# Kernel tuning notes

Measured on AMD Instinct MI355X. Metric: run time of the kernel, lower is better.

The kernel has to match this reference:

```python
import jax, jax.numpy as jnp
import numpy as np

BATCH, N_BEADS, BEAD_SIZE, N_ATOMS = 32, 16384, 16, 100000
INV_SQRT2 = 0.7071067811865476  # e3nn 'uuu' 1o x 1o -> 1e (irrep_normalization='none') cross-product scale


def _mask_arrays():
    # Deterministic bead->atom mask: bead h places count_h = (h % 16) + 1 atoms.
    counts = np.arange(N_BEADS) % BEAD_SIZE + 1
    mask = np.arange(BEAD_SIZE)[None, :] < counts[:, None]  # (n_beads, bead_size)
    slot_idx = np.nonzero(mask.ravel())[0].astype(np.int32)  # flat positions of True entries, (M,)
    bead_idx = np.repeat(np.arange(N_BEADS), counts).astype(np.int32)  # bead id per placed atom, (M,)
    return slot_idx, bead_idx


def setup_inputs() -> dict:
    slot_idx, bead_idx = _mask_arrays()
    M = slot_idx.shape[0]  # 139264
    rng = np.random.default_rng(0)
    atom_idx = rng.integers(0, N_ATOMS, size=M).astype(np.int32)  # bead2atom_idcs flattened over beads
    key = jax.random.key(0)
    kP, k1, k2, kw, ka, ks = jax.random.split(key, 6)
    return {
        'P': jax.random.normal(kP, (BATCH, N_BEADS, 3), jnp.float32),
        'p1': jax.random.normal(k1, (BATCH, N_BEADS, 3), jnp.float32),
        'p2': jax.random.normal(k2, (BATCH, N_BEADS, 3), jnp.float32),
        'weights': jax.random.normal(kw, (3, N_BEADS, BEAD_SIZE), jnp.float32),
        'angles_polar': jax.random.normal(ka, (M, 1), jnp.float32),
        'scaling': jax.random.normal(ks, (N_ATOMS, 1), jnp.float32),
        'slot_idx': jnp.asarray(slot_idx),
        'atom_idx': jnp.asarray(atom_idx),
        'bead_idx': jnp.asarray(bead_idx),
    }


def _q_mult(q1, q2):
    w1, x1, y1, z1 = jnp.moveaxis(q1, -1, 0)
    w2, x2, y2, z2 = jnp.moveaxis(q2, -1, 0)
    w = w1 * w2 - x1 * x2 - y1 * y2 - z1 * z2
    x = w1 * x2 + x1 * w2 + y1 * z2 - z1 * y2
    y = w1 * y2 + y1 * w2 + z1 * x2 - x1 * z2
    z = w1 * z2 + z1 * w2 + x1 * y2 - y1 * x2
    return jnp.stack((w, x, y, z), -1)


def _qv_mult(q, v):
    q2 = jnp.concatenate([jnp.zeros(v.shape[:-1] + (1,), v.dtype), v], -1)
    q_conj = q * jnp.asarray([1.0, -1.0, -1.0, -1.0], q.dtype)
    return _q_mult(_q_mult(q, q2), q_conj)[..., 1:]


def reference(P, p1, p2, weights, angles_polar, scaling, slot_idx, atom_idx, bead_idx):
    B = P.shape[0]
    # per-bead cross product (e3nn TensorProduct 'uuu' path)
    p12 = jnp.cross(p1, p2) * jnp.asarray(INV_SQRT2, p1.dtype)
    stacked = jnp.stack([p1, p2, p12], axis=1)                      # (B, 3, H, 3)
    rot = jnp.einsum('bihk,ihl->bhlk', stacked, weights)            # (B, H, L, 3)
    rot = rot / jnp.linalg.norm(rot, axis=-1, keepdims=True)
    rot_flat = rot.reshape(B, N_BEADS * BEAD_SIZE, 3)[:, slot_idx]  # (B, M, 3) gather via mask
    # quaternions: real = cos(theta), imag = sin(theta) * axis
    cos_a = jnp.cos(angles_polar)                                   # (M, 1)
    sin_a = jnp.sin(angles_polar)
    q = jnp.concatenate([jnp.broadcast_to(cos_a, (B,) + cos_a.shape), sin_a[None] * rot_flat], -1)  # (B, M, 4)
    v = p1[:, bead_idx]                                             # (B, M, 3) repeat_interleave by counts
    v_rot = _qv_mult(q, v)                                          # (B, M, 3)
    recon = scaling[atom_idx][None] * v_rot + P[:, bead_idx]        # (B, M, 3)
    out = jnp.zeros((B, N_ATOMS, 3), P.dtype).at[:, atom_idx].add(recon)  # scatter-add (overlaps accumulate)
    return out, rot_flat.reshape(-1, 3)
```

## Files before the change

kernel.cpp:

```cpp
#include <hip/hip_runtime.h>
#include <hip/hip_fp16.h>
#include <math.h>

#define BATCH   32
#define N_BEADS 16384
#define BEAD_SIZE 16
#define N_ATOMS 100000
#define INV_SQRT2 0.70710678118654752440f
#define SCAN_BLK 256

typedef float v4f __attribute__((ext_vector_type(4)));

__global__ void __launch_bounds__(256)
zero_kernel(int* __restrict__ p, int n)
{
    int i = blockIdx.x * 256 + threadIdx.x;
    if (i < n) p[i] = 0;
}

__global__ void __launch_bounds__(256)
countrec_kernel(const int* __restrict__ atom_idx,
                const int* __restrict__ slot_idx,
                const float* __restrict__ W,
                const float* __restrict__ ang,
                const float* __restrict__ scal,
                int* __restrict__ counts,
                float4* __restrict__ rec1,
                float4* __restrict__ recM2, int M)
{
    int m = blockIdx.x * blockDim.x + threadIdx.x;
    if (m >= M) return;
    int a = atom_idx[m];
    atomicAdd(&counts[a], 1);
    int slot = slot_idx[m];
    int h = slot >> 4, l = slot & 15;
    float w0 = W[(0 * N_BEADS + h) * BEAD_SIZE + l];
    float w1 = W[(1 * N_BEADS + h) * BEAD_SIZE + l];
    float w2 = W[(2 * N_BEADS + h) * BEAD_SIZE + l];
    rec1[m] = make_float4(__int_as_float(slot), w0, w1, w2);
    float sa, ca;
    __sincosf(ang[m], &sa, &ca);
    recM2[m] = make_float4(2.f * ca * sa, 2.f * sa * sa, scal[a], 0.f);
}

__global__ void __launch_bounds__(SCAN_BLK)
scan1_kernel(const int* __restrict__ counts, int* __restrict__ off,
             int* __restrict__ bsum, int n)
{
    __shared__ int s[SCAN_BLK];
    int i = blockIdx.x * SCAN_BLK + threadIdx.x;
    int c = (i < n) ? counts[i] : 0;
    s[threadIdx.x] = c;
    __syncthreads();
    int v = c;
    for (int d = 1; d < SCAN_BLK; d <<= 1) {
        int t = (threadIdx.x >= d) ? s[threadIdx.x - d] : 0;
        __syncthreads();
        v += t;
        s[threadIdx.x] = v;
        __syncthreads();
    }
    if (i < n) off[i] = v - c;
    if (threadIdx.x == SCAN_BLK - 1) bsum[blockIdx.x] = v;
}

__global__ void __launch_bounds__(256)
scan3_kernel(int* __restrict__ off, const int* __restrict__ bsum,
             const int* __restrict__ counts,
             int* __restrict__ cursor2, float4* __restrict__ rec_a, int n)
{
    __shared__ int red[256];
    int j = blockIdx.x;
    int partial = 0;
    for (int i = threadIdx.x; i < j; i += 256) partial += bsum[i];
    red[threadIdx.x] = partial;
    __syncthreads();
    for (int d = 128; d > 0; d >>= 1) {
        if ((int)threadIdx.x < d) red[threadIdx.x] += red[threadIdx.x + d];
        __syncthreads();
    }
    int bpref = red[0];
    int i = j * 256 + threadIdx.x;
    if (i >= n) return;
    int o = off[i] + bpref;
    off[i] = o;
    cursor2[i] = o;
    rec_a[i] = make_float4(__int_as_float(counts[i]), __int_as_float(o),
                           0.f, 0.f);
}

__global__ void __launch_bounds__(256)
fill3_kernel(const int* __restrict__ atom_idx,
             int* __restrict__ cursor2, int* __restrict__ csr_m, int M)
{
    int m = blockIdx.x * blockDim.x + threadIdx.x;
    if (m >= M) return;
    int pos = atomicAdd(&cursor2[atom_idx[m]], 1);
    csr_m[pos] = m;
}

__global__ void __launch_bounds__(256)
mcontrib_kernel(const float4* __restrict__ rec1,
                const float4* __restrict__ recM2,
                const float* __restrict__ p1,
                const float* __restrict__ p2,
                const float* __restrict__ P,
                float* __restrict__ out_rot,
                uint2* __restrict__ cM16,
                int M)
{
    int bg = blockIdx.y;
    int mbase = blockIdx.x * 256;
    int m = mbase + threadIdx.x;
    int b0 = bg * 4;
    bool act = m < M;
    int mc = act ? m : (M - 1);

    float4 r1 = rec1[mc];
    float4 r2 = recM2[mc];
    int h = __float_as_int(r1.x) >> 4;
    float A = r2.x, Bc = r2.y, s = r2.z;
    size_t hoff = (size_t)h * 3;

    __shared__ float sbuf[768];
    int nm = M - mbase; if (nm > 256) nm = 256;
    int nf = nm * 3;
    int nf4 = nf >> 2;
    int done = nf4 << 2;
    int rem = nf - done;

#pragma unroll
    for (int i = 0; i < 4; ++i) {
        int b = b0 + i;
        const size_t bb = (size_t)b * N_BEADS * 3;
        const float* p1p = p1 + bb + hoff;
        const float* p2p = p2 + bb + hoff;
        const float* Pp  = P  + bb + hoff;
        float a1x = p1p[0], a1y = p1p[1], a1z = p1p[2];
        float a2x = p2p[0], a2y = p2p[1], a2z = p2p[2];

        float cxx = (a1y * a2z - a1z * a2y) * INV_SQRT2;
        float cyy = (a1z * a2x - a1x * a2z) * INV_SQRT2;
        float czz = (a1x * a2y - a1y * a2x) * INV_SQRT2;
        float rx = r1.y * a1x + r1.z * a2x + r1.w * cxx;
        float ry = r1.y * a1y + r1.z * a2y + r1.w * cyy;
        float rz = r1.y * a1z + r1.z * a2z + r1.w * czz;
        float inv = rsqrtf(rx * rx + ry * ry + rz * rz);
        rx *= inv; ry *= inv; rz *= inv;

        __syncthreads();
        sbuf[threadIdx.x * 3 + 0] = rx;
        sbuf[threadIdx.x * 3 + 1] = ry;
        sbuf[threadIdx.x * 3 + 2] = rz;
        __syncthreads();
        {
            size_t base = ((size_t)b * M + mbase) * 3;
            v4f* dst = (v4f*)(out_rot + base);
            if ((base & 3) == 0) {
                if ((int)threadIdx.x < nf4)
                    __builtin_nontemporal_store(
                        ((const v4f*)sbuf)[threadIdx.x], &dst[threadIdx.x]);
                if ((int)threadIdx.x < rem)
                    __builtin_nontemporal_store(
                        sbuf[done + threadIdx.x], &out_rot[base + done + threadIdx.x]);
            } else if (act) {
                out_rot[base + threadIdx.x * 3 + 0] = rx;
                out_rot[base + threadIdx.x * 3 + 1] = ry;
                out_rot[base + threadIdx.x * 3 + 2] = rz;
            }
        }

        float ux = ry * a1z - rz * a1y;
        float uy = rz * a1x - rx * a1z;
        float uz = rx * a1y - ry * a1x;
        float wx = ry * uz - rz * uy;
        float wy = rz * ux - rx * uz;
        float wz = rx * uy - ry * ux;
        float ox = s * (a1x + A * ux + Bc * wx) + Pp[0];
        float oy = s * (a1y + A * uy + Bc * wy) + Pp[1];
        float oz = s * (a1z + A * uz + Bc * wz) + Pp[2];

        if (act) {
            union { struct { __half2 lo, hi; } hh; uint2 u; } pk;
            pk.hh.lo = __floats2half2_rn(ox, oy);
            pk.hh.hi = __floats2half2_rn(oz, 0.f);
            cM16[(size_t)b * M + m] = pk.u;
        }
    }
}

__global__ void __launch_bounds__(256)
sum2_kernel(const float4* __restrict__ rec_a,
            const int* __restrict__ csr_m,
            const uint2* __restrict__ cM16,
            float* __restrict__ out_atoms, int M, int abps)
{
    int beta = blockIdx.x;
    int xcd  = beta & 7;
    int j    = beta >> 3;
    int round = j / abps;
    int ablk  = j - round * abps;
    int b = xcd + 8 * round;
    int abase = ablk * 256;
    int a = abase + threadIdx.x;

    float ax = 0.f, ay = 0.f, az = 0.f;
    if (a < N_ATOMS) {
        float4 ra = rec_a[a];
        int cnt = __float_as_int(ra.x);
        int o   = __float_as_int(ra.y);
        const uint2* cb = cM16 + (size_t)b * M;
        for (int k = 0; k < cnt; ++k) {
            int m = csr_m[o + k];
            union { uint2 u; struct { __half2 lo, hi; } hh; } pk;
            pk.u = cb[m];
            float2 xy = __half22float2(pk.hh.lo);
            float2 zp = __half22float2(pk.hh.hi);
            ax += xy.x; ay += xy.y; az += zp.x;
        }
    }
    __shared__ float sbuf[768];
    sbuf[threadIdx.x * 3 + 0] = ax;
    sbuf[threadIdx.x * 3 + 1] = ay;
    sbuf[threadIdx.x * 3 + 2] = az;
    __syncthreads();

    int na = N_ATOMS - abase; if (na > 256) na = 256;
    int nf = na * 3;
    size_t base = ((size_t)b * N_ATOMS + abase) * 3;
    int nf4 = nf >> 2;
    v4f* dst = (v4f*)(out_atoms + base);
    if ((int)threadIdx.x < nf4)
        __builtin_nontemporal_store(((const v4f*)sbuf)[threadIdx.x],
                                    &dst[threadIdx.x]);
    int done = nf4 << 2;
    int rem = nf - done;
    if ((int)threadIdx.x < rem)
        __builtin_nontemporal_store(sbuf[done + threadIdx.x],
                                    &out_atoms[base + done + threadIdx.x]);
}

__global__ void __launch_bounds__(256)
backmap_fallback(const float* __restrict__ P, const float* __restrict__ p1,
                 const float* __restrict__ p2, const float* __restrict__ W,
                 const float* __restrict__ ang, const float* __restrict__ scal,
                 const int* __restrict__ slot_idx, const int* __restrict__ atom_idx,
                 float* __restrict__ out_atoms, float* __restrict__ out_rot, int M)
{
    int t = blockIdx.x * blockDim.x + threadIdx.x;
    if (t >= BATCH * M) return;
    int b = t / M; int m = t - b * M;
    int slot = slot_idx[m]; int h = slot >> 4; int l = slot & 15;
    int atom = atom_idx[m];
    const float* p1p = p1 + ((size_t)b * N_BEADS + h) * 3;
    const float* p2p = p2 + ((size_t)b * N_BEADS + h) * 3;
    float a1x = p1p[0], a1y = p1p[1], a1z = p1p[2];
    float a2x = p2p[0], a2y = p2p[1], a2z = p2p[2];
    float cx = (a1y * a2z - a1z * a2y) * INV_SQRT2;
    float cy = (a1z * a2x - a1x * a2z) * INV_SQRT2;
    float cz = (a1x * a2y - a1y * a2x) * INV_SQRT2;
    float w0 = W[(0 * N_BEADS + h) * BEAD_SIZE + l];
    float w1 = W[(1 * N_BEADS + h) * BEAD_SIZE + l];
    float w2 = W[(2 * N_BEADS + h) * BEAD_SIZE + l];
    float rx = w0 * a1x + w1 * a2x + w2 * cx;
    float ry = w0 * a1y + w1 * a2y + w2 * cy;
    float rz = w0 * a1z + w1 * a2z + w2 * cz;
    float inv = rsqrtf(rx * rx + ry * ry + rz * rz);
    rx *= inv; ry *= inv; rz *= inv;
    float* ro = out_rot + (size_t)t * 3;
    ro[0] = rx; ro[1] = ry; ro[2] = rz;
    float sa, ca; __sincosf(ang[m], &sa, &ca);
    float A = 2.f * ca * sa, Bc = 2.f * sa * sa;
    float ux = ry * a1z - rz * a1y;
    float uy = rz * a1x - rx * a1z;
    float uz = rx * a1y - ry * a1x;
    float wx = ry * uz - rz * uy;
    float wy = rz * ux - rx * uz;
    float wz = rx * uy - ry * ux;
    float s = scal[atom];
    const float* Pp = P + ((size_t)b * N_BEADS + h) * 3;
    float* op = out_atoms + ((size_t)b * N_ATOMS + atom) * 3;
    atomicAdd(op + 0, s * (a1x + A * ux + Bc * wx) + Pp[0]);
    atomicAdd(op + 1, s * (a1y + A * uy + Bc * wy) + Pp[1]);
    atomicAdd(op + 2, s * (a1z + A * uz + Bc * wz) + Pp[2]);
}

extern "C" void kernel_launch(void* const* d_in, const int* in_sizes, int n_in,
                              void* d_out, int out_size, void* d_ws, size_t ws_size,
                              hipStream_t stream) {
    const float* P    = (const float*)d_in[0];
    const float* p1   = (const float*)d_in[1];
    const float* p2   = (const float*)d_in[2];
    const float* W    = (const float*)d_in[3];
    const float* ang  = (const float*)d_in[4];
    const float* scal = (const float*)d_in[5];
    const int* slot_idx = (const int*)d_in[6];
    const int* atom_idx = (const int*)d_in[7];

    int M = in_sizes[6];
    float* out_atoms = (float*)d_out;
    float* out_rot   = out_atoms + (size_t)BATCH * N_ATOMS * 3;

    int nblk   = (N_ATOMS + SCAN_BLK - 1) / SCAN_BLK;
    int nchunk = (M + 255) / 256;

    size_t intpre = (size_t)N_ATOMS * 4 * 3 + 512 * 4;
    size_t need   = intpre + (size_t)M * 16 * 2 + (size_t)N_ATOMS * 16
                  + (size_t)M * 4 + (size_t)BATCH * M * 8;

    if (ws_size >= need) {
        int* counts  = (int*)d_ws;
        int* off     = counts + N_ATOMS;
        int* cursor2 = off + N_ATOMS;
        int* bsum    = cursor2 + N_ATOMS;
        float4* rec1  = (float4*)((char*)d_ws + intpre);
        float4* recM2 = rec1 + M;
        float4* rec_a = recM2 + M;
        int*    csr_m = (int*)(rec_a + N_ATOMS);
        uint2*  cM16  = (uint2*)(csr_m + M);

        zero_kernel<<<nblk, 256, 0, stream>>>(counts, N_ATOMS);
        countrec_kernel<<<nchunk, 256, 0, stream>>>(
            atom_idx, slot_idx, W, ang, scal, counts, rec1, recM2, M);
        scan1_kernel<<<nblk, SCAN_BLK, 0, stream>>>(counts, off, bsum, N_ATOMS);
        scan3_kernel<<<nblk, 256, 0, stream>>>(off, bsum, counts,
                                               cursor2, rec_a, N_ATOMS);
        fill3_kernel<<<nchunk, 256, 0, stream>>>(atom_idx, cursor2, csr_m, M);

        dim3 gm(nchunk, 8);
        mcontrib_kernel<<<gm, 256, 0, stream>>>(
            rec1, recM2, p1, p2, P, out_rot, cM16, M);

        int abps = (N_ATOMS + 255) / 256;
        sum2_kernel<<<abps * BATCH, 256, 0, stream>>>(
            rec_a, csr_m, cM16, out_atoms, M, abps);
        return;
    }

    hipMemsetAsync(out_atoms, 0, (size_t)BATCH * N_ATOMS * 3 * sizeof(float), stream);
    int total = BATCH * M;
    backmap_fallback<<<(total + 255) / 256, 256, 0, stream>>>(
        P, p1, p2, W, ang, scal, slot_idx, atom_idx,
        out_atoms, out_rot, M);
}
```

Before: 90.90 us.

## Split rotation-output writes out of contribution kernel into separate rot kernel

Splits the fused kernel in two. One kernel computes the half-precision per-atom contributions with no shared-memory staging and no barriers. A separate rot_kernel, launched after the scatter-sum, recomputes the normalized rotation vectors and writes out_rot using coalesced nontemporal stores. This removes the barriers and out_rot traffic from the contribution path, at the cost of reading p1 and p2 again, redoing the cross products, and one extra kernel launch.

```diff
diff --git a/kernel.cpp b/kernel.cpp
--- a/kernel.cpp
+++ b/kernel.cpp
@@ -100,34 +100,24 @@
 }
 
 __global__ void __launch_bounds__(256)
-mcontrib_kernel(const float4* __restrict__ rec1,
-                const float4* __restrict__ recM2,
-                const float* __restrict__ p1,
-                const float* __restrict__ p2,
-                const float* __restrict__ P,
-                float* __restrict__ out_rot,
-                uint2* __restrict__ cM16,
-                int M)
+contrib16_kernel(const float4* __restrict__ rec1,
+                 const float4* __restrict__ recM2,
+                 const float* __restrict__ p1,
+                 const float* __restrict__ p2,
+                 const float* __restrict__ P,
+                 uint2* __restrict__ cM16,
+                 int M)
 {
     int bg = blockIdx.y;
-    int mbase = blockIdx.x * 256;
-    int m = mbase + threadIdx.x;
+    int m = blockIdx.x * 256 + threadIdx.x;
+    if (m >= M) return;
     int b0 = bg * 4;
-    bool act = m < M;
-    int mc = act ? m : (M - 1);
-
-    float4 r1 = rec1[mc];
-    float4 r2 = recM2[mc];
+
+    float4 r1 = rec1[m];
+    float4 r2 = recM2[m];
     int h = __float_as_int(r1.x) >> 4;
     float A = r2.x, Bc = r2.y, s = r2.z;
     size_t hoff = (size_t)h * 3;
-
-    __shared__ float sbuf[768];
-    int nm = M - mbase; if (nm > 256) nm = 256;
-    int nf = nm * 3;
-    int nf4 = nf >> 2;
-    int done = nf4 << 2;
-    int rem = nf - done;
 
 #pragma unroll
     for (int i = 0; i < 4; ++i) {
@@ -148,28 +138,6 @@
         float inv = rsqrtf(rx * rx + ry * ry + rz * rz);
         rx *= inv; ry *= inv; rz *= inv;
 
-        __syncthreads();
-        sbuf[threadIdx.x * 3 + 0] = rx;
-        sbuf[threadIdx.x * 3 + 1] = ry;
-        sbuf[threadIdx.x * 3 + 2] = rz;
-        __syncthreads();
-        {
-            size_t base = ((size_t)b * M + mbase) * 3;
-            v4f* dst = (v4f*)(out_rot + base);
-            if ((base & 3) == 0) {
-                if ((int)threadIdx.x < nf4)
-                    __builtin_nontemporal_store(
-                        ((const v4f*)sbuf)[threadIdx.x], &dst[threadIdx.x]);
-                if ((int)threadIdx.x < rem)
-                    __builtin_nontemporal_store(
-                        sbuf[done + threadIdx.x], &out_rot[base + done + threadIdx.x]);
-            } else if (act) {
-                out_rot[base + threadIdx.x * 3 + 0] = rx;
-                out_rot[base + threadIdx.x * 3 + 1] = ry;
-                out_rot[base + threadIdx.x * 3 + 2] = rz;
-            }
-        }
-
         float ux = ry * a1z - rz * a1y;
         float uy = rz * a1x - rx * a1z;
         float uz = rx * a1y - ry * a1x;
@@ -180,12 +148,64 @@
         float oy = s * (a1y + A * uy + Bc * wy) + Pp[1];
         float oz = s * (a1z + A * uz + Bc * wz) + Pp[2];
 
-        if (act) {
-            union { struct { __half2 lo, hi; } hh; uint2 u; } pk;
-            pk.hh.lo = __floats2half2_rn(ox, oy);
-            pk.hh.hi = __floats2half2_rn(oz, 0.f);
-            cM16[(size_t)b * M + m] = pk.u;
-        }
+        union { struct { __half2 lo, hi; } hh; uint2 u; } pk;
+        pk.hh.lo = __floats2half2_rn(ox, oy);
+        pk.hh.hi = __floats2half2_rn(oz, 0.f);
+        cM16[(size_t)b * M + m] = pk.u;
+    }
+}
+
+__global__ void __launch_bounds__(256)
+rot_kernel(const float4* __restrict__ rec1,
+           const float* __restrict__ p1,
+           const float* __restrict__ p2,
+           float* __restrict__ out_rot, int M)
+{
+    int b = blockIdx.y;
+    int mbase = blockIdx.x * 256;
+    int m = mbase + threadIdx.x;
+    __shared__ float sbuf[768];
+
+    float rx = 0.f, ry = 0.f, rz = 0.f;
+    if (m < M) {
+        float4 r1 = rec1[m];
+        int h = __float_as_int(r1.x) >> 4;
+        const float* p1p = p1 + ((size_t)b * N_BEADS + h) * 3;
+        const float* p2p = p2 + ((size_t)b * N_BEADS + h) * 3;
+        float a1x = p1p[0], a1y = p1p[1], a1z = p1p[2];
+        float a2x = p2p[0], a2y = p2p[1], a2z = p2p[2];
+        float cxx = (a1y * a2z - a1z * a2y) * INV_SQRT2;
+        float cyy = (a1z * a2x - a1x * a2z) * INV_SQRT2;
+        float czz = (a1x * a2y - a1y * a2x) * INV_SQRT2;
+        rx = r1.y * a1x + r1.z * a2x + r1.w * cxx;
+        ry = r1.y * a1y + r1.z * a2y + r1.w * cyy;
+        rz = r1.y * a1z + r1.z * a2z + r1.w * czz;
+        float inv = rsqrtf(rx * rx + ry * ry + rz * rz);
+        rx *= inv; ry *= inv; rz *= inv;
+    }
+    sbuf[threadIdx.x * 3 + 0] = rx;
+    sbuf[threadIdx.x * 3 + 1] = ry;
+    sbuf[threadIdx.x * 3 + 2] = rz;
+    __syncthreads();
+
+    int nm = M - mbase; if (nm > 256) nm = 256;
+    int nf = nm * 3;
+    size_t base = ((size_t)b * M + mbase) * 3;
+    if ((base & 3) == 0) {
+        int nf4 = nf >> 2;
+        v4f* dst = (v4f*)(out_rot + base);
+        if ((int)threadIdx.x < nf4)
+            __builtin_nontemporal_store(((const v4f*)sbuf)[threadIdx.x],
+                                        &dst[threadIdx.x]);
+        int done = nf4 << 2;
+        int rem = nf - done;
+        if ((int)threadIdx.x < rem)
+            __builtin_nontemporal_store(sbuf[done + threadIdx.x],
+                                        &out_rot[base + done + threadIdx.x]);
+    } else if (m < M) {
+        out_rot[base + threadIdx.x * 3 + 0] = rx;
+        out_rot[base + threadIdx.x * 3 + 1] = ry;
+        out_rot[base + threadIdx.x * 3 + 2] = rz;
     }
 }
 
@@ -327,13 +347,16 @@
                                                cursor2, rec_a, N_ATOMS);
         fill3_kernel<<<nchunk, 256, 0, stream>>>(atom_idx, cursor2, csr_m, M);
 
-        dim3 gm(nchunk, 8);
-        mcontrib_kernel<<<gm, 256, 0, stream>>>(
-            rec1, recM2, p1, p2, P, out_rot, cM16, M);
+        dim3 gc(nchunk, 8);
+        contrib16_kernel<<<gc, 256, 0, stream>>>(
+            rec1, recM2, p1, p2, P, cM16, M);
 
         int abps = (N_ATOMS + 255) / 256;
         sum2_kernel<<<abps * BATCH, 256, 0, stream>>>(
             rec_a, csr_m, cM16, out_atoms, M, abps);
+
+        dim3 gr(nchunk, BATCH);
+        rot_kernel<<<gr, 256, 0, stream>>>(rec1, p1, p2, out_rot, M);
         return;
     }
 
```

After: 99.52 us. 1.09x slower.
